# Optimization experiments

Measured on AMD Instinct MI355X. Metric: run time of the kernel, lower is better.

The kernel has to match this reference:

```python
import jax, jax.numpy as jnp
import numpy as np

K = 5  # k_neighbors


def _pairwise_sq(a, b):
    # (B,N,3),(B,M,3) -> (B,N,M) squared euclidean distances (matmul form)
    d = (jnp.sum(a * a, -1)[:, :, None] + jnp.sum(b * b, -1)[:, None, :]
         - 2.0 * jnp.einsum('bnd,bmd->bnm', a, b))
    return jnp.maximum(d, 0.0)


def _knn_indices(points, k):
    # (B,N,3) -> (B,N,k) indices of k nearest neighbors, excluding self
    d = _pairwise_sq(points, points)
    _, idx = jax.lax.top_k(-d, k + 1)
    return idx[:, :, 1:]


def _gather_neighbors(feats, idx):
    # feats (B,N,C), idx (B,N,k) -> (B,N,k,C)
    B, N, k = idx.shape
    flat = jnp.take_along_axis(feats, idx.reshape(B, N * k, 1), axis=1)
    return flat.reshape(B, N, k, feats.shape[-1])


def setup_inputs() -> dict:
    key = jax.random.key(0)
    ks = jax.random.split(key, 8)
    B, N, M = 8, 4096, 4000
    return {
        'Y': jax.random.normal(ks[0], (B, N, 3), jnp.float32),
        'X': jax.random.normal(ks[1], (B, M, 3), jnp.float32),
        'R_pred': jax.random.normal(ks[2], (B, 3, 3), jnp.float32),
        't_pred': jax.random.normal(ks[3], (B, 3), jnp.float32),
        'R_gt': jax.random.normal(ks[4], (B, 3, 3), jnp.float32),
        't_gt': jax.random.normal(ks[5], (B, 3), jnp.float32),
        'X_hat': jax.random.normal(ks[6], (B, N, 3), jnp.float32),
        'delta': jax.random.normal(ks[7], (B, N, 3), jnp.float32),
    }


def reference(Y, X, R_pred, t_pred, R_gt, t_gt, X_hat, delta):
    lam_rot, lam_trans, lam_rmse = 1.0, 1.0, 1.0
    lam_align, lam_disp, lam_deform, lam_lap = 1.0, 0.01, 0.1, 0.1

    # --- rigid losses ---
    # rotation geodesic: R_delta = R_pred^T @ R_gt
    R_delta = jnp.einsum('bij,bik->bjk', R_pred, R_gt)
    tr = jnp.trace(R_delta, axis1=1, axis2=2)
    cos_a = jnp.clip((tr - 1.0) / 2.0, -1.0 + 1e-7, 1.0 - 1e-7)
    L_rot = jnp.mean(jnp.arccos(cos_a))

    L_trans = jnp.mean(jnp.linalg.norm(t_pred - t_gt, axis=1))

    # Y @ R^T + t
    Y_pred = jnp.einsum('bnd,bkd->bnk', Y, R_pred) + t_pred[:, None, :]
    Y_gt = jnp.einsum('bnd,bkd->bnk', Y, R_gt) + t_gt[:, None, :]
    L_rmse = jnp.mean(jnp.sqrt(jnp.mean(jnp.sum((Y_pred - Y_gt) ** 2, -1), axis=1)))

    rigid = lam_rot * L_rot + lam_trans * L_trans + lam_rmse * L_rmse

    # --- non-rigid losses ---
    Y_rigid = Y_pred  # apply_rigid_transform(Y, R_pred, t_pred)

    # alignment: N != M -> kNN matching of X_hat against X
    d_align = _pairwise_sq(X_hat, X)          # (B,N,M)
    knn_d = -jax.lax.top_k(-d_align, K)[0]    # (B,N,K) smallest distances
    L_align = jnp.mean(knn_d)

    L_disp = jnp.mean(jnp.sum(delta ** 2, -1))

    # kNN graph on Y_rigid (original builds it twice with identical result)
    idx = _knn_indices(Y_rigid, K)            # (B,N,K)

    Yn = _gather_neighbors(Y_rigid, idx)      # (B,N,K,3)
    Xn = _gather_neighbors(X_hat, idx)
    edge_diff = (Xn - X_hat[:, :, None, :]) - (Yn - Y_rigid[:, :, None, :])
    L_deform = jnp.mean(jnp.sum(edge_diff ** 2, -1))

    dn = _gather_neighbors(delta, idx)        # (B,N,K,3)
    lap = delta - jnp.mean(dn, axis=2)
    L_lap = jnp.mean(jnp.sum(lap ** 2, -1))

    non_rigid = (lam_align * L_align + lam_disp * L_disp
                 + lam_deform * L_deform + lam_lap * L_lap)
    total = rigid + non_rigid

    return jnp.stack([total, rigid, non_rigid, L_rot, L_trans, L_rmse,
                      L_align, L_disp, L_deform, L_lap])
```

## Files before the change

kernel.cpp:

```cpp
#include <hip/hip_runtime.h>
#include <math.h>

#define BB 8
#define NN 4096
#define MM 4000
#define KK 5
#define NWAVE 8
#define QG 128
#define CH 256
#define HSZ 2048
#define NPAD 4096
#define SCAN_BLOCKS ((NN / QG) * BB * 2)

#define ACC_ROT    0
#define ACC_TRANS  1
#define ACC_ALIGN  2
#define ACC_DISP   3
#define ACC_DEFORM 4
#define ACC_LAP    5
#define ACC_RMSE   6
#define ACC_COUNT  14

#define INFF __int_as_float(0x7F800000)

__device__ __forceinline__ float waveReduceSum(float v) {
#pragma unroll
    for (int off = 32; off > 0; off >>= 1) v += __shfl_down(v, off, 64);
    return v;
}

template<bool SELF, bool PACK>
__device__ __forceinline__ void proc1(float4 c, int midx, int q,
                                      float ca, float cbq, float cc,
                                      float& b0, float& b1, float& b2,
                                      float& b3, float& b4) {
    float sc = fmaf(c.x, ca, fmaf(c.y, cbq, fmaf(c.z, cc, c.w)));
    float v;
    if (PACK) {
        unsigned pk = (__float_as_uint(sc) & 0xFFFFF000u) | (unsigned)midx;
        v = __uint_as_float(pk);
        if (SELF) v = (midx == q) ? INFF : v;
    } else {
        v = sc;
    }
    float n0 = fminf(b0, v);
    float n1 = __builtin_amdgcn_fmed3f(v, b0, b1);
    float n2 = __builtin_amdgcn_fmed3f(v, b1, b2);
    float n3 = __builtin_amdgcn_fmed3f(v, b2, b3);
    float n4 = __builtin_amdgcn_fmed3f(v, b3, b4);
    b0 = n0; b1 = n1; b2 = n2; b3 = n3; b4 = n4;
}

template<bool SELF, bool PACK>
__device__ __forceinline__ void scanLDS2(const float4* lc, int tl, int tg,
                                         float a0, float b0c, float c0, int q0,
                                         float a1, float b1c, float c1, int q1,
                                         float& x0, float& x1, float& x2,
                                         float& x3, float& x4,
                                         float& y0, float& y1, float& y2,
                                         float& y3, float& y4) {
    float4 A[4], B[4];
#pragma unroll
    for (int j = 0; j < 4; ++j) A[j] = lc[tl + j];

    for (int t0 = 0; t0 < CH; t0 += 8) {
#pragma unroll
        for (int j = 0; j < 4; ++j) B[j] = lc[tl + t0 + 4 + j];
#pragma unroll
        for (int j = 0; j < 4; ++j) {
            proc1<SELF, PACK>(A[j], tg + t0 + j, q0, a0, b0c, c0, x0, x1, x2, x3, x4);
            proc1<SELF, PACK>(A[j], tg + t0 + j, q1, a1, b1c, c1, y0, y1, y2, y3, y4);
        }
        if (t0 + 8 < CH) {
#pragma unroll
            for (int j = 0; j < 4; ++j) A[j] = lc[tl + t0 + 8 + j];
        }
#pragma unroll
        for (int j = 0; j < 4; ++j) {
            proc1<SELF, PACK>(B[j], tg + t0 + 4 + j, q0, a0, b0c, c0, x0, x1, x2, x3, x4);
            proc1<SELF, PACK>(B[j], tg + t0 + 4 + j, q1, a1, b1c, c1, y0, y1, y2, y3, y4);
        }
    }
}

__device__ __forceinline__ void merge5(float& a0, float& a1, float& a2,
                                       float& a3, float& a4,
                                       float m0, float m1, float m2,
                                       float m3, float m4) {
    float u0 = fminf(a0, m0);
    float u1 = fminf(fminf(a1, m1), fmaxf(a0, m0));
    float u2 = fminf(fminf(a2, m2), fminf(fmaxf(a0, m1), fmaxf(a1, m0)));
    float u3 = fminf(fminf(a3, m3),
                     fminf(fmaxf(a0, m2), fminf(fmaxf(a1, m1), fmaxf(a2, m0))));
    float u4 = fminf(fminf(a4, m4),
                     fminf(fminf(fmaxf(a0, m3), fmaxf(a1, m2)),
                           fminf(fmaxf(a2, m1), fmaxf(a3, m0))));
    a0 = u0; a1 = u1; a2 = u2; a3 = u3; a4 = u4;
}

__global__ void k_prep(const float* __restrict__ Y, const float* __restrict__ X,
                       const float* __restrict__ Rp, const float* __restrict__ tp,
                       const float* __restrict__ Rg, const float* __restrict__ tg,
                       const float* __restrict__ dl,
                       float4* __restrict__ YrP, float4* __restrict__ XP,
                       float* __restrict__ acc) {
    int b = blockIdx.x >> 4;
    int n = ((blockIdx.x & 15) << 8) + threadIdx.x;
    size_t base = ((size_t)b * NN + n) * 3;
    float yx = Y[base + 0], yy = Y[base + 1], yz = Y[base + 2];

    float rp[9], rg[9], tpv[3], tgv[3];
#pragma unroll
    for (int i = 0; i < 9; ++i) { rp[i] = Rp[b * 9 + i]; rg[i] = Rg[b * 9 + i]; }
#pragma unroll
    for (int i = 0; i < 3; ++i) { tpv[i] = tp[b * 3 + i]; tgv[i] = tg[b * 3 + i]; }

    float p[3], dr2 = 0.f;
#pragma unroll
    for (int k = 0; k < 3; ++k) {
        float pv = fmaf(yx, rp[k * 3 + 0], fmaf(yy, rp[k * 3 + 1], fmaf(yz, rp[k * 3 + 2], tpv[k])));
        float gv = fmaf(yx, rg[k * 3 + 0], fmaf(yy, rg[k * 3 + 1], fmaf(yz, rg[k * 3 + 2], tgv[k])));
        p[k] = pv;
        float dd = pv - gv;
        dr2 = fmaf(dd, dd, dr2);
    }
    YrP[(size_t)b * NPAD + n] =
        make_float4(p[0], p[1], p[2], fmaf(p[0], p[0], fmaf(p[1], p[1], p[2] * p[2])));

    float4 xe;
    if (n < MM) {
        size_t xb = ((size_t)b * MM + n) * 3;
        float x0 = X[xb + 0], x1 = X[xb + 1], x2 = X[xb + 2];
        xe = make_float4(x0, x1, x2, fmaf(x0, x0, fmaf(x1, x1, x2 * x2)));
    } else {
        xe = make_float4(0.f, 0.f, 0.f, INFF);
    }
    XP[(size_t)b * NPAD + n] = xe;

    float d0 = dl[base + 0], d1 = dl[base + 1], d2 = dl[base + 2];
    float dsq = d0 * d0 + d1 * d1 + d2 * d2;

    dr2 = waveReduceSum(dr2);
    dsq = waveReduceSum(dsq);
    if ((threadIdx.x & 63) == 0) {
        atomicAdd(&acc[ACC_RMSE + b], dr2);
        atomicAdd(&acc[ACC_DISP], dsq);
    }

    if (threadIdx.x == 0 && (blockIdx.x & 15) == 0) {
        float tr = 0.f;
#pragma unroll
        for (int i = 0; i < 9; ++i) tr += rp[i] * rg[i];
        float c = (tr - 1.f) * 0.5f;
        c = fminf(fmaxf(c, -1.f + 1e-7f), 1.f - 1e-7f);
        float dx = tpv[0] - tgv[0], dy = tpv[1] - tgv[1], dz = tpv[2] - tgv[2];
        atomicAdd(&acc[ACC_ROT], acosf(c));
        atomicAdd(&acc[ACC_TRANS], sqrtf(dx * dx + dy * dy + dz * dz));
    }
}

__device__ void finalize(const float* acc, float* out) {
    float a[ACC_COUNT];
#pragma unroll
    for (int i = 0; i < ACC_COUNT; ++i)
        a[i] = __hip_atomic_load(&acc[i], __ATOMIC_RELAXED, __HIP_MEMORY_SCOPE_AGENT);
    float L_rot = a[ACC_ROT] / BB;
    float L_trans = a[ACC_TRANS] / BB;
    float L_rmse = 0.f;
#pragma unroll
    for (int b = 0; b < BB; ++b) L_rmse += sqrtf(a[ACC_RMSE + b] / NN);
    L_rmse /= BB;
    float L_align = a[ACC_ALIGN] / ((float)BB * NN * KK);
    float L_disp = a[ACC_DISP] / ((float)BB * NN);
    float L_def = a[ACC_DEFORM] / ((float)BB * NN * KK);
    float L_lap = a[ACC_LAP] / ((float)BB * NN);
    float rigid = L_rot + L_trans + L_rmse;
    float nr = L_align + 0.01f * L_disp + 0.1f * L_def + 0.1f * L_lap;
    out[0] = rigid + nr; out[1] = rigid; out[2] = nr;
    out[3] = L_rot; out[4] = L_trans; out[5] = L_rmse;
    out[6] = L_align; out[7] = L_disp; out[8] = L_def; out[9] = L_lap;
}

#define MERGE_STEP(W) { float d = md[W][l][pp##W]; if (d < best) { best = d; bw = W; } }
#define MERGE_ADV()  { pp0 += (bw == 0); pp1 += (bw == 1); pp2 += (bw == 2); pp3 += (bw == 3); \
                       pp4 += (bw == 4); pp5 += (bw == 5); pp6 += (bw == 6); pp7 += (bw == 7); }

__global__ __launch_bounds__(512, 4) void k_scan(const float* __restrict__ Xh,
                                                 const float4* __restrict__ XP,
                                                 const float4* __restrict__ YrP,
                                                 const float* __restrict__ dl,
                                                 float* __restrict__ acc,
                                                 unsigned* __restrict__ doneCnt,
                                                 float* __restrict__ out) {
    __shared__ float4 stage[HSZ];
    __shared__ float md[NWAVE][QG][6];
    int tid = threadIdx.x, wave = tid >> 6, lane = tid & 63;
    int qg = blockIdx.x, b = blockIdx.y, mode = blockIdx.z;
    int q0 = qg * QG + lane, q1 = q0 + 64;

    const float4* cbG = (mode == 0 ? XP : YrP) + (size_t)b * NPAD;

    float qx0, qy0, qz0, qx1, qy1, qz1;
    if (mode == 0) {
        size_t a0 = ((size_t)b * NN + q0) * 3;
        size_t a1 = ((size_t)b * NN + q1) * 3;
        qx0 = Xh[a0 + 0]; qy0 = Xh[a0 + 1]; qz0 = Xh[a0 + 2];
        qx1 = Xh[a1 + 0]; qy1 = Xh[a1 + 1]; qz1 = Xh[a1 + 2];
    } else {
        float4 p0 = cbG[q0], p1 = cbG[q1];
        qx0 = p0.x; qy0 = p0.y; qz0 = p0.z;
        qx1 = p1.x; qy1 = p1.y; qz1 = p1.z;
    }

    float f0 = INFF, f1 = INFF, f2 = INFF, f3 = INFF, f4 = INFF;

#pragma unroll
    for (int half = 0; half < 2; ++half) {
        __syncthreads();
#pragma unroll
        for (int i = 0; i < HSZ / 512; ++i)
            stage[tid + i * 512] = cbG[half * HSZ + tid + i * 512];
        __syncthreads();

        float x0 = INFF, x1 = INFF, x2 = INFF, x3 = INFF, x4 = INFF;
        float y0 = INFF, y1 = INFF, y2 = INFF, y3 = INFF, y4 = INFF;
        int tl = wave * CH;
        int tg = half * HSZ + tl;
        bool hasSelf = (mode == 1) && (half == (qg >> 4)) && (wave == ((qg >> 1) & 7));
        if (mode == 0) {
            scanLDS2<false, false>(stage, tl, tg,
                                   -2.f * qx0, -2.f * qy0, -2.f * qz0, 0,
                                   -2.f * qx1, -2.f * qy1, -2.f * qz1, 0,
                                   x0, x1, x2, x3, x4, y0, y1, y2, y3, y4);
        } else if (hasSelf) {
            scanLDS2<true, true>(stage, tl, tg,
                                 -2.f * qx0, -2.f * qy0, -2.f * qz0, q0,
                                 -2.f * qx1, -2.f * qy1, -2.f * qz1, q1,
                                 x0, x1, x2, x3, x4, y0, y1, y2, y3, y4);
        } else {
            scanLDS2<false, true>(stage, tl, tg,
                                  -2.f * qx0, -2.f * qy0, -2.f * qz0, q0,
                                  -2.f * qx1, -2.f * qy1, -2.f * qz1, q1,
                                  x0, x1, x2, x3, x4, y0, y1, y2, y3, y4);
        }

        md[wave][lane][0] = x0; md[wave][lane][1] = x1; md[wave][lane][2] = x2;
        md[wave][lane][3] = x3; md[wave][lane][4] = x4; md[wave][lane][5] = INFF;
        md[wave][lane + 64][0] = y0; md[wave][lane + 64][1] = y1;
        md[wave][lane + 64][2] = y2; md[wave][lane + 64][3] = y3;
        md[wave][lane + 64][4] = y4; md[wave][lane + 64][5] = INFF;
        __syncthreads();

        if (tid < QG) {
            int l = tid;
            int pp0 = 0, pp1 = 0, pp2 = 0, pp3 = 0, pp4 = 0, pp5 = 0, pp6 = 0, pp7 = 0;
            float m5[KK];
#pragma unroll
            for (int k = 0; k < KK; ++k) {
                float best = INFF; int bw = 0;
                MERGE_STEP(0) MERGE_STEP(1) MERGE_STEP(2) MERGE_STEP(3)
                MERGE_STEP(4) MERGE_STEP(5) MERGE_STEP(6) MERGE_STEP(7)
                m5[k] = best;
                MERGE_ADV()
            }
            merge5(f0, f1, f2, f3, f4, m5[0], m5[1], m5[2], m5[3], m5[4]);
        }
    }

    if (tid < QG) {
        int l = tid;
        int q = qg * QG + l;
        if (mode == 0) {
            size_t a0 = ((size_t)b * NN + q) * 3;
            float qx = Xh[a0 + 0], qy = Xh[a0 + 1], qz = Xh[a0 + 2];
            float qn = fmaf(qx, qx, fmaf(qy, qy, qz * qz));
            float s = fmaxf(f0 + qn, 0.f) + fmaxf(f1 + qn, 0.f) + fmaxf(f2 + qn, 0.f)
                    + fmaxf(f3 + qn, 0.f) + fmaxf(f4 + qn, 0.f);
            s = waveReduceSum(s);
            if ((l & 63) == 0) atomicAdd(&acc[ACC_ALIGN], s);
        } else {
            int si[KK];
            si[0] = (int)(__float_as_uint(f0) & 0xFFFu);
            si[1] = (int)(__float_as_uint(f1) & 0xFFFu);
            si[2] = (int)(__float_as_uint(f2) & 0xFFFu);
            si[3] = (int)(__float_as_uint(f3) & 0xFFFu);
            si[4] = (int)(__float_as_uint(f4) & 0xFFFu);

            float4 qp = cbG[q];
            const float* xh = Xh + (size_t)b * NN * 3;
            const float* dlb = dl + (size_t)b * NN * 3;
            float xnx = xh[q * 3 + 0], xny = xh[q * 3 + 1], xnz = xh[q * 3 + 2];
            float dnx = dlb[q * 3 + 0], dny = dlb[q * 3 + 1], dnz = dlb[q * 3 + 2];

            float def = 0.f, sx = 0.f, sy = 0.f, sz = 0.f;
#pragma unroll
            for (int k = 0; k < KK; ++k) {
                int n = si[k];
                float4 yj = cbG[n];
                float ex = (xh[n * 3 + 0] - xnx) - (yj.x - qp.x);
                float ey = (xh[n * 3 + 1] - xny) - (yj.y - qp.y);
                float ez = (xh[n * 3 + 2] - xnz) - (yj.z - qp.z);
                def += ex * ex + ey * ey + ez * ez;
                sx += dlb[n * 3 + 0]; sy += dlb[n * 3 + 1]; sz += dlb[n * 3 + 2];
            }
            float lx = dnx - sx / 5.f, ly = dny - sy / 5.f, lz = dnz - sz / 5.f;
            float lap = lx * lx + ly * ly + lz * lz;

            def = waveReduceSum(def);
            lap = waveReduceSum(lap);
            if ((l & 63) == 0) {
                atomicAdd(&acc[ACC_DEFORM], def);
                atomicAdd(&acc[ACC_LAP], lap);
            }
        }
    }
    __syncthreads();
    if (tid == 0) {
        __threadfence();
        unsigned t = __hip_atomic_fetch_add(doneCnt, 1u, __ATOMIC_ACQ_REL,
                                            __HIP_MEMORY_SCOPE_AGENT);
        if (t == SCAN_BLOCKS - 1) finalize(acc, out);
    }
}

extern "C" void kernel_launch(void* const* d_in, const int* in_sizes, int n_in,
                              void* d_out, int out_size, void* d_ws, size_t ws_size,
                              hipStream_t stream) {
    const float* Y  = (const float*)d_in[0];
    const float* X  = (const float*)d_in[1];
    const float* Rp = (const float*)d_in[2];
    const float* tp = (const float*)d_in[3];
    const float* Rg = (const float*)d_in[4];
    const float* tg = (const float*)d_in[5];
    const float* Xh = (const float*)d_in[6];
    const float* dl = (const float*)d_in[7];
    float* out = (float*)d_out;

    float*    acc     = (float*)d_ws;
    unsigned* doneCnt = (unsigned*)((char*)d_ws + 64);
    float4*   YrP     = (float4*)((char*)d_ws + 512);
    float4*   XP      = YrP + (size_t)BB * NPAD;

    hipMemsetAsync(d_ws, 0, 512, stream);
    hipLaunchKernelGGL(k_prep, dim3(BB * NN / 256), dim3(256), 0, stream,
                       Y, X, Rp, tp, Rg, tg, dl, YrP, XP, acc);
    hipLaunchKernelGGL(k_scan, dim3(NN / QG, BB, 2), dim3(512), 0, stream,
                       Xh, XP, YrP, dl, acc, doneCnt, out);
}
```

Before: 108.4 us.

## Process four queries per thread in kNN scan to raise LDS reuse

Each thread now keeps four independent top-5 chains instead of two, and the query group per block doubles to 256. Every candidate point loaded from LDS is reused across four distance evaluations, which halves LDS traffic per comparison and adds instruction-level parallelism. The cost is more registers, a larger shared merge buffer, and half as many blocks. That can lower occupancy under launch_bounds(512,4), and the grid may underfill the GPU.

```diff
diff --git a/kernel.cpp b/kernel.cpp
--- a/kernel.cpp
+++ b/kernel.cpp
@@ -6,7 +6,7 @@
 #define MM 4000
 #define KK 5
 #define NWAVE 8
-#define QG 128
+#define QG 256
 #define CH 256
 #define HSZ 2048
 #define NPAD 4096
@@ -23,6 +23,8 @@
 
 #define INFF __int_as_float(0x7F800000)
 
+struct Chain { float b0, b1, b2, b3, b4; };
+
 __device__ __forceinline__ float waveReduceSum(float v) {
 #pragma unroll
     for (int off = 32; off > 0; off >>= 1) v += __shfl_down(v, off, 64);
@@ -31,9 +33,7 @@
 
 template<bool SELF, bool PACK>
 __device__ __forceinline__ void proc1(float4 c, int midx, int q,
-                                      float ca, float cbq, float cc,
-                                      float& b0, float& b1, float& b2,
-                                      float& b3, float& b4) {
+                                      float ca, float cbq, float cc, Chain& h) {
     float sc = fmaf(c.x, ca, fmaf(c.y, cbq, fmaf(c.z, cc, c.w)));
     float v;
     if (PACK) {
@@ -43,22 +43,20 @@
     } else {
         v = sc;
     }
-    float n0 = fminf(b0, v);
-    float n1 = __builtin_amdgcn_fmed3f(v, b0, b1);
-    float n2 = __builtin_amdgcn_fmed3f(v, b1, b2);
-    float n3 = __builtin_amdgcn_fmed3f(v, b2, b3);
-    float n4 = __builtin_amdgcn_fmed3f(v, b3, b4);
-    b0 = n0; b1 = n1; b2 = n2; b3 = n3; b4 = n4;
+    float n0 = fminf(h.b0, v);
+    float n1 = __builtin_amdgcn_fmed3f(v, h.b0, h.b1);
+    float n2 = __builtin_amdgcn_fmed3f(v, h.b1, h.b2);
+    float n3 = __builtin_amdgcn_fmed3f(v, h.b2, h.b3);
+    float n4 = __builtin_amdgcn_fmed3f(v, h.b3, h.b4);
+    h.b0 = n0; h.b1 = n1; h.b2 = n2; h.b3 = n3; h.b4 = n4;
 }
 
 template<bool SELF, bool PACK>
-__device__ __forceinline__ void scanLDS2(const float4* lc, int tl, int tg,
-                                         float a0, float b0c, float c0, int q0,
-                                         float a1, float b1c, float c1, int q1,
-                                         float& x0, float& x1, float& x2,
-                                         float& x3, float& x4,
-                                         float& y0, float& y1, float& y2,
-                                         float& y3, float& y4) {
+__device__ __forceinline__ void scanLDS4(const float4* lc, int tl, int tg,
+                                         float a0, float e0, float c0, int q0, Chain& C0,
+                                         float a1, float e1, float c1, int q1, Chain& C1,
+                                         float a2, float e2, float c2, int q2, Chain& C2,
+                                         float a3, float e3, float c3, int q3, Chain& C3) {
     float4 A[4], B[4];
 #pragma unroll
     for (int j = 0; j < 4; ++j) A[j] = lc[tl + j];
@@ -68,8 +66,11 @@
         for (int j = 0; j < 4; ++j) B[j] = lc[tl + t0 + 4 + j];
 #pragma unroll
         for (int j = 0; j < 4; ++j) {
-            proc1<SELF, PACK>(A[j], tg + t0 + j, q0, a0, b0c, c0, x0, x1, x2, x3, x4);
-            proc1<SELF, PACK>(A[j], tg + t0 + j, q1, a1, b1c, c1, y0, y1, y2, y3, y4);
+            int m = tg + t0 + j;
+            proc1<SELF, PACK>(A[j], m, q0, a0, e0, c0, C0);
+            proc1<SELF, PACK>(A[j], m, q1, a1, e1, c1, C1);
+            proc1<SELF, PACK>(A[j], m, q2, a2, e2, c2, C2);
+            proc1<SELF, PACK>(A[j], m, q3, a3, e3, c3, C3);
         }
         if (t0 + 8 < CH) {
 #pragma unroll
@@ -77,8 +78,11 @@
         }
 #pragma unroll
         for (int j = 0; j < 4; ++j) {
-            proc1<SELF, PACK>(B[j], tg + t0 + 4 + j, q0, a0, b0c, c0, x0, x1, x2, x3, x4);
-            proc1<SELF, PACK>(B[j], tg + t0 + 4 + j, q1, a1, b1c, c1, y0, y1, y2, y3, y4);
+            int m = tg + t0 + 4 + j;
+            proc1<SELF, PACK>(B[j], m, q0, a0, e0, c0, C0);
+            proc1<SELF, PACK>(B[j], m, q1, a1, e1, c1, C1);
+            proc1<SELF, PACK>(B[j], m, q2, a2, e2, c2, C2);
+            proc1<SELF, PACK>(B[j], m, q3, a3, e3, c3, C3);
         }
     }
 }
@@ -196,20 +200,26 @@
     __shared__ float md[NWAVE][QG][6];
     int tid = threadIdx.x, wave = tid >> 6, lane = tid & 63;
     int qg = blockIdx.x, b = blockIdx.y, mode = blockIdx.z;
-    int q0 = qg * QG + lane, q1 = q0 + 64;
+    int q0 = qg * QG + lane, q1 = q0 + 64, q2 = q0 + 128, q3 = q0 + 192;
 
     const float4* cbG = (mode == 0 ? XP : YrP) + (size_t)b * NPAD;
 
-    float qx0, qy0, qz0, qx1, qy1, qz1;
+    float ax0, ay0, az0, ax1, ay1, az1, ax2, ay2, az2, ax3, ay3, az3;
     if (mode == 0) {
         size_t a0 = ((size_t)b * NN + q0) * 3;
         size_t a1 = ((size_t)b * NN + q1) * 3;
-        qx0 = Xh[a0 + 0]; qy0 = Xh[a0 + 1]; qz0 = Xh[a0 + 2];
-        qx1 = Xh[a1 + 0]; qy1 = Xh[a1 + 1]; qz1 = Xh[a1 + 2];
+        size_t a2 = ((size_t)b * NN + q2) * 3;
+        size_t a3 = ((size_t)b * NN + q3) * 3;
+        ax0 = Xh[a0 + 0]; ay0 = Xh[a0 + 1]; az0 = Xh[a0 + 2];
+        ax1 = Xh[a1 + 0]; ay1 = Xh[a1 + 1]; az1 = Xh[a1 + 2];
+        ax2 = Xh[a2 + 0]; ay2 = Xh[a2 + 1]; az2 = Xh[a2 + 2];
+        ax3 = Xh[a3 + 0]; ay3 = Xh[a3 + 1]; az3 = Xh[a3 + 2];
     } else {
-        float4 p0 = cbG[q0], p1 = cbG[q1];
-        qx0 = p0.x; qy0 = p0.y; qz0 = p0.z;
-        qx1 = p1.x; qy1 = p1.y; qz1 = p1.z;
+        float4 p0 = cbG[q0], p1 = cbG[q1], p2 = cbG[q2], p3 = cbG[q3];
+        ax0 = p0.x; ay0 = p0.y; az0 = p0.z;
+        ax1 = p1.x; ay1 = p1.y; az1 = p1.z;
+        ax2 = p2.x; ay2 = p2.y; az2 = p2.z;
+        ax3 = p3.x; ay3 = p3.y; az3 = p3.z;
     }
 
     float f0 = INFF, f1 = INFF, f2 = INFF, f3 = INFF, f4 = INFF;
@@ -222,33 +232,42 @@
             stage[tid + i * 512] = cbG[half * HSZ + tid + i * 512];
         __syncthreads();
 
-        float x0 = INFF, x1 = INFF, x2 = INFF, x3 = INFF, x4 = INFF;
-        float y0 = INFF, y1 = INFF, y2 = INFF, y3 = INFF, y4 = INFF;
+        Chain C0 = { INFF, INFF, INFF, INFF, INFF };
+        Chain C1 = { INFF, INFF, INFF, INFF, INFF };
+        Chain C2 = { INFF, INFF, INFF, INFF, INFF };
+        Chain C3 = { INFF, INFF, INFF, INFF, INFF };
         int tl = wave * CH;
         int tg = half * HSZ + tl;
-        bool hasSelf = (mode == 1) && (half == (qg >> 4)) && (wave == ((qg >> 1) & 7));
+        bool hasSelf = (mode == 1) && (half == (qg >> 3)) && (wave == (qg & 7));
         if (mode == 0) {
-            scanLDS2<false, false>(stage, tl, tg,
-                                   -2.f * qx0, -2.f * qy0, -2.f * qz0, 0,
-                                   -2.f * qx1, -2.f * qy1, -2.f * qz1, 0,
-                                   x0, x1, x2, x3, x4, y0, y1, y2, y3, y4);
+            scanLDS4<false, false>(stage, tl, tg,
+                                   -2.f * ax0, -2.f * ay0, -2.f * az0, 0, C0,
+                                   -2.f * ax1, -2.f * ay1, -2.f * az1, 0, C1,
+                                   -2.f * ax2, -2.f * ay2, -2.f * az2, 0, C2,
+                                   -2.f * ax3, -2.f * ay3, -2.f * az3, 0, C3);
         } else if (hasSelf) {
-            scanLDS2<true, true>(stage, tl, tg,
-                                 -2.f * qx0, -2.f * qy0, -2.f * qz0, q0,
-                                 -2.f * qx1, -2.f * qy1, -2.f * qz1, q1,
-                                 x0, x1, x2, x3, x4, y0, y1, y2, y3, y4);
+            scanLDS4<true, true>(stage, tl, tg,
+                                 -2.f * ax0, -2.f * ay0, -2.f * az0, q0, C0,
+                                 -2.f * ax1, -2.f * ay1, -2.f * az1, q1, C1,
+                                 -2.f * ax2, -2.f * ay2, -2.f * az2, q2, C2,
+                                 -2.f * ax3, -2.f * ay3, -2.f * az3, q3, C3);
         } else {
-            scanLDS2<false, true>(stage, tl, tg,
-                                  -2.f * qx0, -2.f * qy0, -2.f * qz0, q0,
-                                  -2.f * qx1, -2.f * qy1, -2.f * qz1, q1,
-                                  x0, x1, x2, x3, x4, y0, y1, y2, y3, y4);
-        }
-
-        md[wave][lane][0] = x0; md[wave][lane][1] = x1; md[wave][lane][2] = x2;
-        md[wave][lane][3] = x3; md[wave][lane][4] = x4; md[wave][lane][5] = INFF;
-        md[wave][lane + 64][0] = y0; md[wave][lane + 64][1] = y1;
-        md[wave][lane + 64][2] = y2; md[wave][lane + 64][3] = y3;
-        md[wave][lane + 64][4] = y4; md[wave][lane + 64][5] = INFF;
+            scanLDS4<false, true>(stage, tl, tg,
+                                  -2.f * ax0, -2.f * ay0, -2.f * az0, q0, C0,
+                                  -2.f * ax1, -2.f * ay1, -2.f * az1, q1, C1,
+                                  -2.f * ax2, -2.f * ay2, -2.f * az2, q2, C2,
+                                  -2.f * ax3, -2.f * ay3, -2.f * az3, q3, C3);
+        }
+
+        float* m;
+        m = &md[wave][lane][0];
+        m[0] = C0.b0; m[1] = C0.b1; m[2] = C0.b2; m[3] = C0.b3; m[4] = C0.b4; m[5] = INFF;
+        m = &md[wave][lane + 64][0];
+        m[0] = C1.b0; m[1] = C1.b1; m[2] = C1.b2; m[3] = C1.b3; m[4] = C1.b4; m[5] = INFF;
+        m = &md[wave][lane + 128][0];
+        m[0] = C2.b0; m[1] = C2.b1; m[2] = C2.b2; m[3] = C2.b3; m[4] = C2.b4; m[5] = INFF;
+        m = &md[wave][lane + 192][0];
+        m[0] = C3.b0; m[1] = C3.b1; m[2] = C3.b2; m[3] = C3.b3; m[4] = C3.b4; m[5] = INFF;
         __syncthreads();
 
         if (tid < QG) {
```

Measured after the change: 118.9 us. +9.7%, slower.
